# Performance work log

Hardware: AMD Instinct MI355X
Metric: run time of the kernel (lower is better)

The kernel has to match this reference:

```python
import jax, jax.numpy as jnp
import numpy as np

N, D, K = 262144, 64, 512


def setup_inputs() -> dict:
    key = jax.random.key(0)
    k1, k2 = jax.random.split(key)
    x = jax.random.normal(k1, (N, D), dtype=jnp.float32)
    # embedding initialized uniform(-1/K, 1/K) as in the torch module
    codebook = jax.random.uniform(k2, (K, D), dtype=jnp.float32, minval=-1.0 / K, maxval=1.0 / K)
    return {"x": x, "codebook": codebook}


def reference(x, codebook):
    # distances[n,k] = ||x_n||^2 + ||w_k||^2 - 2 x_n . w_k  (cdist^2 via matmul)
    d = (jnp.sum(x * x, axis=1, keepdims=True)
         + jnp.sum(codebook * codebook, axis=1)
         - 2.0 * jnp.matmul(x, codebook.T))  # [N, K]
    indices = jnp.argmin(d, axis=1)          # [N]
    x_q = codebook[indices]                  # [N, D] gather
    commitment_loss = jnp.mean((jax.lax.stop_gradient(x_q) - x) ** 2)
    embedding_loss = jnp.mean((x_q - jax.lax.stop_gradient(x)) ** 2)
    vq_loss = commitment_loss * 0.25 + embedding_loss
    # straight-through estimator
    x_out = x + jax.lax.stop_gradient(x_q - x)
    return (x_out, vq_loss)
```

## Files before the change

kernel.cpp:

```cpp
#include <hip/hip_runtime.h>
#include <hip/hip_bf16.h>
#include <hip/hip_fp8.h>

#define N_ROWS 262144
#define DIM    64
#define KCB    512

#define BLOCKS  1024
#define THREADS 512

typedef float f32x4 __attribute__((ext_vector_type(4)));

__device__ inline float dot4(float4 a) {
    return a.x * a.x + a.y * a.y + a.z * a.z + a.w * a.w;
}
__device__ inline unsigned umin2(unsigned a, unsigned b) { return a < b ? a : b; }

__device__ inline unsigned pk4(float a, float b, float c, float d) {
    unsigned r;
    r  = (unsigned)__hip_fp8_e4m3(a).__x;
    r |= (unsigned)__hip_fp8_e4m3(b).__x << 8;
    r |= (unsigned)__hip_fp8_e4m3(c).__x << 16;
    r |= (unsigned)__hip_fp8_e4m3(d).__x << 24;
    return r;
}
__device__ inline long pk8(float4 f0, float4 f1, float s) {
    unsigned lo = pk4(f0.x * s, f0.y * s, f0.z * s, f0.w * s);
    unsigned hi = pk4(f1.x * s, f1.y * s, f1.z * s, f1.w * s);
    return (long)(((unsigned long)hi << 32) | (unsigned long)lo);
}

__global__ __launch_bounds__(THREADS, 2) void vq_main(
    const float* __restrict__ x, const float* __restrict__ cb,
    float* __restrict__ out, float* __restrict__ partials)
{
    __shared__ long   cb8_sh[KCB * 8];
    __shared__ f32x4  wn_sh4[KCB / 4];
    __shared__ float  red_sh[8];

    const int tid    = threadIdx.x;
    const int lane   = tid & 63;
    const int wave   = tid >> 6;
    const int lane15 = lane & 15;
    const int half   = lane >> 4;

    const int wrow = blockIdx.x * 256 + wave * 32;
    const float* xc0 = x + (size_t)(wrow + lane15) * DIM + half * 8;
    const float* xc1 = x + (size_t)(wrow + 16 + lane15) * DIM + half * 8;

    float4 p00 = *(const float4*)xc0,        p01 = *(const float4*)(xc0 + 4);
    float4 p02 = *(const float4*)(xc0 + 32), p03 = *(const float4*)(xc0 + 36);
    float4 p10 = *(const float4*)xc1,        p11 = *(const float4*)(xc1 + 4);
    float4 p12 = *(const float4*)(xc1 + 32), p13 = *(const float4*)(xc1 + 36);

    #pragma unroll
    for (int it = 0; it < (KCB * 8) / THREADS; ++it) {
        const int fg = tid + it * THREADS;
        const int row = fg >> 3, g = fg & 7;
        const float* src = cb + row * DIM + g * 8;
        float4 f0 = *(const float4*)src;
        float4 f1 = *(const float4*)(src + 4);
        float sq = dot4(f0) + dot4(f1);
        sq += __shfl_xor(sq, 1);
        sq += __shfl_xor(sq, 2);
        sq += __shfl_xor(sq, 4);
        const int slot = ((row >> 1) << 4) + ((row & 1) << 3)
                       + (g ^ ((row >> 1) & 7));
        cb8_sh[slot] = pk8(f0, f1, -256.0f);
        if (g == 0) ((float*)wn_sh4)[row] = 256.0f + 128.0f * sq;
    }

    float xn0 = dot4(p00) + dot4(p01) + dot4(p02) + dot4(p03);
    float xn1 = dot4(p10) + dot4(p11) + dot4(p12) + dot4(p13);
    long b0lo = pk8(p00, p01, 1.0f), b0hi = pk8(p02, p03, 1.0f);
    long b1lo = pk8(p10, p11, 1.0f), b1hi = pk8(p12, p13, 1.0f);
    __syncthreads();

    const int key  = (lane15 >> 1) & 7;
    const int base = (lane15 >> 1) * 16 + (lane15 & 1) * 8;
    const int slo  = base + (half ^ key);
    const int shi  = slo ^ 4;
    const unsigned hb = (unsigned)(half * 4);

    unsigned u0 = 0xFFFFFFFFu, u1 = 0xFFFFFFFFu;

    #pragma unroll 8
    for (int t = 0; t < 32; ++t) {
        long  alo = cb8_sh[t * 128 + slo];
        long  ahi = cb8_sh[t * 128 + shi];
        f32x4 wnv = wn_sh4[t * 4 + half];
        const unsigned kb = (unsigned)(t * 16) | hb;

        f32x4 acc = wnv;
        acc = __builtin_amdgcn_mfma_f32_16x16x32_fp8_fp8(alo, b0lo, acc, 0, 0, 0);
        acc = __builtin_amdgcn_mfma_f32_16x16x32_fp8_fp8(ahi, b0hi, acc, 0, 0, 0);
        unsigned p0 = (__float_as_uint(acc[0]) & 0xFFFFFE00u) | kb;
        unsigned p1 = (__float_as_uint(acc[1]) & 0xFFFFFE00u) | (kb | 1u);
        unsigned p2 = (__float_as_uint(acc[2]) & 0xFFFFFE00u) | (kb | 2u);
        unsigned p3 = (__float_as_uint(acc[3]) & 0xFFFFFE00u) | (kb | 3u);
        u0 = umin2(u0, umin2(umin2(p0, p1), umin2(p2, p3)));

        f32x4 acd = wnv;
        acd = __builtin_amdgcn_mfma_f32_16x16x32_fp8_fp8(alo, b1lo, acd, 0, 0, 0);
        acd = __builtin_amdgcn_mfma_f32_16x16x32_fp8_fp8(ahi, b1hi, acd, 0, 0, 0);
        unsigned r0 = (__float_as_uint(acd[0]) & 0xFFFFFE00u) | kb;
        unsigned r1 = (__float_as_uint(acd[1]) & 0xFFFFFE00u) | (kb | 1u);
        unsigned r2 = (__float_as_uint(acd[2]) & 0xFFFFFE00u) | (kb | 2u);
        unsigned r3 = (__float_as_uint(acd[3]) & 0xFFFFFE00u) | (kb | 3u);
        u1 = umin2(u1, umin2(umin2(r0, r1), umin2(r2, r3)));
    }

    unsigned f0 = u0;
    f0 = umin2(f0, (unsigned)__shfl_xor((int)f0, 16));
    f0 = umin2(f0, (unsigned)__shfl_xor((int)f0, 32));
    unsigned f1 = u1;
    f1 = umin2(f1, (unsigned)__shfl_xor((int)f1, 16));
    f1 = umin2(f1, (unsigned)__shfl_xor((int)f1, 32));

    float xs0 = xn0;
    xs0 += __shfl_xor(xs0, 16); xs0 += __shfl_xor(xs0, 32);
    float xs1 = xn1;
    xs1 += __shfl_xor(xs1, 16); xs1 += __shfl_xor(xs1, 32);

    float pf0 = __uint_as_float(f0 & 0xFFFFFE00u);
    float pf1 = __uint_as_float(f1 & 0xFFFFFE00u);
    float lossAcc = 0.25f * (xs0 + pf0 * (1.0f / 128.0f) - 2.0f)
                  + 0.25f * (xs1 + pf1 * (1.0f / 128.0f) - 2.0f);

    const int bk0 = (int)(f0 & 511u);
    const int bk1 = (int)(f1 & 511u);

    float* outw = out + (size_t)wrow * DIM;
    #pragma unroll
    for (int j = 0; j < 8; ++j) {
        const int srcl = (j * 4 + half) & 15;
        int bk = __shfl((j >> 2) ? bk1 : bk0, srcl);
        float4 qv = *(const float4*)(cb + (size_t)bk * DIM + (lane & 15) * 4);
        *(float4*)(outw + j * 256 + lane * 4) = qv;
    }

    #pragma unroll
    for (int off = 1; off < 64; off <<= 1) lossAcc += __shfl_xor(lossAcc, off);
    if (lane == 0) red_sh[wave] = lossAcc;
    __syncthreads();
    if (tid == 0) {
        float s = 0.f;
        #pragma unroll
        for (int w = 0; w < 8; ++w) s += red_sh[w];
        partials[blockIdx.x] = s;
    }
}

__global__ void vq_finalize(const float* __restrict__ partials,
                            float* __restrict__ out_loss) {
    __shared__ float sh[256];
    int t = threadIdx.x;
    sh[t] = partials[t] + partials[t + 256] + partials[t + 512] + partials[t + 768];
    __syncthreads();
    #pragma unroll
    for (int s = 128; s > 0; s >>= 1) {
        if (t < s) sh[t] += sh[t + s];
        __syncthreads();
    }
    if (t == 0) out_loss[0] = sh[0] * (1.25f / (float)(N_ROWS * DIM));
}

extern "C" void kernel_launch(void* const* d_in, const int* in_sizes, int n_in,
                              void* d_out, int out_size, void* d_ws, size_t ws_size,
                              hipStream_t stream) {
    const float* x  = (const float*)d_in[0];
    const float* cb = (const float*)d_in[1];
    float* out      = (float*)d_out;
    float* partials = (float*)d_ws;

    hipLaunchKernelGGL(vq_main, dim3(BLOCKS), dim3(THREADS), 0, stream,
                       x, cb, out, partials);
    hipLaunchKernelGGL(vq_finalize, dim3(1), dim3(256), 0, stream,
                       partials, out + (size_t)N_ROWS * DIM);
}
```

Baseline: 44.80 us.

## Split VQ into score kernel writing indices and separate gather kernel

The fused kernel is split in two. The scoring kernel now writes only 16-bit argmin indices to workspace, and a new lightweight gather kernel writes the quantized rows to the output. The scoring loop handles its two 16-row chunks one after the other instead of interleaved, which lowers register pressure, and the second chunk's x loads are issued after the barrier so they overlap with the first chunk's compute. FP8 packing now uses the cvt_pk_fp8_f32 builtin. The cost is an extra kernel launch and an extra pass over the index buffer, plus less instruction-level parallelism in the MFMA loop.

```diff
diff --git a/kernel.cpp b/kernel.cpp
--- a/kernel.cpp
+++ b/kernel.cpp
@@ -1,13 +1,13 @@
 #include <hip/hip_runtime.h>
-#include <hip/hip_bf16.h>
-#include <hip/hip_fp8.h>
 
 #define N_ROWS 262144
 #define DIM    64
 #define KCB    512
 
-#define BLOCKS  1024
-#define THREADS 512
+#define ABLOCKS  1024
+#define ATHREADS 512
+#define BTHREADS 256
+#define BBLOCKS  ((N_ROWS * 16) / BTHREADS)
 
 typedef float f32x4 __attribute__((ext_vector_type(4)));
 
@@ -16,23 +16,18 @@
 }
 __device__ inline unsigned umin2(unsigned a, unsigned b) { return a < b ? a : b; }
 
-__device__ inline unsigned pk4(float a, float b, float c, float d) {
-    unsigned r;
-    r  = (unsigned)__hip_fp8_e4m3(a).__x;
-    r |= (unsigned)__hip_fp8_e4m3(b).__x << 8;
-    r |= (unsigned)__hip_fp8_e4m3(c).__x << 16;
-    r |= (unsigned)__hip_fp8_e4m3(d).__x << 24;
-    return r;
-}
 __device__ inline long pk8(float4 f0, float4 f1, float s) {
-    unsigned lo = pk4(f0.x * s, f0.y * s, f0.z * s, f0.w * s);
-    unsigned hi = pk4(f1.x * s, f1.y * s, f1.z * s, f1.w * s);
-    return (long)(((unsigned long)hi << 32) | (unsigned long)lo);
+    int lo = 0, hi = 0;
+    lo = __builtin_amdgcn_cvt_pk_fp8_f32(f0.x * s, f0.y * s, lo, false);
+    lo = __builtin_amdgcn_cvt_pk_fp8_f32(f0.z * s, f0.w * s, lo, true);
+    hi = __builtin_amdgcn_cvt_pk_fp8_f32(f1.x * s, f1.y * s, hi, false);
+    hi = __builtin_amdgcn_cvt_pk_fp8_f32(f1.z * s, f1.w * s, hi, true);
+    return (long)(((unsigned long)(unsigned)hi << 32) | (unsigned)lo);
 }
 
-__global__ __launch_bounds__(THREADS, 2) void vq_main(
+__global__ __launch_bounds__(ATHREADS, 2) void vq_score(
     const float* __restrict__ x, const float* __restrict__ cb,
-    float* __restrict__ out, float* __restrict__ partials)
+    unsigned short* __restrict__ idx, float* __restrict__ partials)
 {
     __shared__ long   cb8_sh[KCB * 8];
     __shared__ f32x4  wn_sh4[KCB / 4];
@@ -45,17 +40,14 @@
     const int half   = lane >> 4;
 
     const int wrow = blockIdx.x * 256 + wave * 32;
-    const float* xc0 = x + (size_t)(wrow + lane15) * DIM + half * 8;
-    const float* xc1 = x + (size_t)(wrow + 16 + lane15) * DIM + half * 8;
+    const float* xc = x + (size_t)(wrow + lane15) * DIM + half * 8;
 
-    float4 p00 = *(const float4*)xc0,        p01 = *(const float4*)(xc0 + 4);
-    float4 p02 = *(const float4*)(xc0 + 32), p03 = *(const float4*)(xc0 + 36);
-    float4 p10 = *(const float4*)xc1,        p11 = *(const float4*)(xc1 + 4);
-    float4 p12 = *(const float4*)(xc1 + 32), p13 = *(const float4*)(xc1 + 36);
+    float4 p00 = *(const float4*)xc,        p01 = *(const float4*)(xc + 4);
+    float4 p02 = *(const float4*)(xc + 32), p03 = *(const float4*)(xc + 36);
 
     #pragma unroll
-    for (int it = 0; it < (KCB * 8) / THREADS; ++it) {
-        const int fg = tid + it * THREADS;
+    for (int it = 0; it < (KCB * 8) / ATHREADS; ++it) {
+        const int fg = tid + it * ATHREADS;
         const int row = fg >> 3, g = fg & 7;
         const float* src = cb + row * DIM + g * 8;
         float4 f0 = *(const float4*)src;
@@ -71,72 +63,59 @@
     }
 
     float xn0 = dot4(p00) + dot4(p01) + dot4(p02) + dot4(p03);
-    float xn1 = dot4(p10) + dot4(p11) + dot4(p12) + dot4(p13);
     long b0lo = pk8(p00, p01, 1.0f), b0hi = pk8(p02, p03, 1.0f);
-    long b1lo = pk8(p10, p11, 1.0f), b1hi = pk8(p12, p13, 1.0f);
     __syncthreads();
+
+    float4 q00 = *(const float4*)(xc + 1024), q01 = *(const float4*)(xc + 1028);
+    float4 q02 = *(const float4*)(xc + 1056), q03 = *(const float4*)(xc + 1060);
 
     const int key  = (lane15 >> 1) & 7;
     const int base = (lane15 >> 1) * 16 + (lane15 & 1) * 8;
     const int slo  = base + (half ^ key);
     const int shi  = slo ^ 4;
-    const unsigned hb = (unsigned)(half * 4);
+    const unsigned hb   = (unsigned)(half * 4);
+    const unsigned mask = 0xFFFFFE00u;
 
-    unsigned u0 = 0xFFFFFFFFu, u1 = 0xFFFFFFFFu;
+    float lossAcc = 0.f;
+    long blo = b0lo, bhi = b0hi;
+    float xn = xn0;
 
-    #pragma unroll 8
-    for (int t = 0; t < 32; ++t) {
-        long  alo = cb8_sh[t * 128 + slo];
-        long  ahi = cb8_sh[t * 128 + shi];
-        f32x4 wnv = wn_sh4[t * 4 + half];
-        const unsigned kb = (unsigned)(t * 16) | hb;
+    #pragma unroll
+    for (int ch = 0; ch < 2; ++ch) {
+        if (ch == 1) {
+            xn  = dot4(q00) + dot4(q01) + dot4(q02) + dot4(q03);
+            blo = pk8(q00, q01, 1.0f);
+            bhi = pk8(q02, q03, 1.0f);
+        }
+        unsigned u0 = 0xFFFFFFFFu;
 
-        f32x4 acc = wnv;
-        acc = __builtin_amdgcn_mfma_f32_16x16x32_fp8_fp8(alo, b0lo, acc, 0, 0, 0);
-        acc = __builtin_amdgcn_mfma_f32_16x16x32_fp8_fp8(ahi, b0hi, acc, 0, 0, 0);
-        unsigned p0 = (__float_as_uint(acc[0]) & 0xFFFFFE00u) | kb;
-        unsigned p1 = (__float_as_uint(acc[1]) & 0xFFFFFE00u) | (kb | 1u);
-        unsigned p2 = (__float_as_uint(acc[2]) & 0xFFFFFE00u) | (kb | 2u);
-        unsigned p3 = (__float_as_uint(acc[3]) & 0xFFFFFE00u) | (kb | 3u);
-        u0 = umin2(u0, umin2(umin2(p0, p1), umin2(p2, p3)));
+        #pragma unroll 8
+        for (int t = 0; t < 32; ++t) {
+            long  alo = cb8_sh[t * 128 + slo];
+            long  ahi = cb8_sh[t * 128 + shi];
+            f32x4 wnv = wn_sh4[t * 4 + half];
+            const unsigned kb = (unsigned)(t * 16) | hb;
 
-        f32x4 acd = wnv;
-        acd = __builtin_amdgcn_mfma_f32_16x16x32_fp8_fp8(alo, b1lo, acd, 0, 0, 0);
-        acd = __builtin_amdgcn_mfma_f32_16x16x32_fp8_fp8(ahi, b1hi, acd, 0, 0, 0);
-        unsigned r0 = (__float_as_uint(acd[0]) & 0xFFFFFE00u) | kb;
-        unsigned r1 = (__float_as_uint(acd[1]) & 0xFFFFFE00u) | (kb | 1u);
-        unsigned r2 = (__float_as_uint(acd[2]) & 0xFFFFFE00u) | (kb | 2u);
-        unsigned r3 = (__float_as_uint(acd[3]) & 0xFFFFFE00u) | (kb | 3u);
-        u1 = umin2(u1, umin2(umin2(r0, r1), umin2(r2, r3)));
-    }
+            f32x4 acc = wnv;
+            acc = __builtin_amdgcn_mfma_f32_16x16x32_fp8_fp8(alo, blo, acc, 0, 0, 0);
+            acc = __builtin_amdgcn_mfma_f32_16x16x32_fp8_fp8(ahi, bhi, acc, 0, 0, 0);
+            unsigned p0 = (__float_as_uint(acc[0]) & mask) | kb;
+            unsigned p1 = (__float_as_uint(acc[1]) & mask) | (kb | 1u);
+            unsigned p2 = (__float_as_uint(acc[2]) & mask) | (kb | 2u);
+            unsigned p3 = (__float_as_uint(acc[3]) & mask) | (kb | 3u);
+            u0 = umin2(u0, umin2(umin2(p0, p1), umin2(p2, p3)));
+        }
 
-    unsigned f0 = u0;
-    f0 = umin2(f0, (unsigned)__shfl_xor((int)f0, 16));
-    f0 = umin2(f0, (unsigned)__shfl_xor((int)f0, 32));
-    unsigned f1 = u1;
-    f1 = umin2(f1, (unsigned)__shfl_xor((int)f1, 16));
-    f1 = umin2(f1, (unsigned)__shfl_xor((int)f1, 32));
+        unsigned f0 = u0;
+        f0 = umin2(f0, (unsigned)__shfl_xor((int)f0, 16));
+        f0 = umin2(f0, (unsigned)__shfl_xor((int)f0, 32));
+        float xs = xn;
+        xs += __shfl_xor(xs, 16); xs += __shfl_xor(xs, 32);
 
-    float xs0 = xn0;
-    xs0 += __shfl_xor(xs0, 16); xs0 += __shfl_xor(xs0, 32);
-    float xs1 = xn1;
-    xs1 += __shfl_xor(xs1, 16); xs1 += __shfl_xor(xs1, 32);
+        float pf = __uint_as_float(f0 & mask);
+        lossAcc += 0.25f * (xs + pf * (1.0f / 128.0f) - 2.0f);
 
-    float pf0 = __uint_as_float(f0 & 0xFFFFFE00u);
-    float pf1 = __uint_as_float(f1 & 0xFFFFFE00u);
-    float lossAcc = 0.25f * (xs0 + pf0 * (1.0f / 128.0f) - 2.0f)
-                  + 0.25f * (xs1 + pf1 * (1.0f / 128.0f) - 2.0f);
-
-    const int bk0 = (int)(f0 & 511u);
-    const int bk1 = (int)(f1 & 511u);
-
-    float* outw = out + (size_t)wrow * DIM;
-    #pragma unroll
-    for (int j = 0; j < 8; ++j) {
-        const int srcl = (j * 4 + half) & 15;
-        int bk = __shfl((j >> 2) ? bk1 : bk0, srcl);
-        float4 qv = *(const float4*)(cb + (size_t)bk * DIM + (lane & 15) * 4);
-        *(float4*)(outw + j * 256 + lane * 4) = qv;
+        if (lane < 16) idx[wrow + ch * 16 + lane] = (unsigned short)(f0 & 511u);
     }
 
     #pragma unroll
@@ -149,6 +128,18 @@
         for (int w = 0; w < 8; ++w) s += red_sh[w];
         partials[blockIdx.x] = s;
     }
+}
+
+__global__ __launch_bounds__(BTHREADS, 8) void vq_gather(
+    const unsigned short* __restrict__ idx, const float* __restrict__ cb,
+    float* __restrict__ out)
+{
+    const int g   = blockIdx.x * BTHREADS + threadIdx.x;
+    const int row = g >> 4;
+    const int dq  = g & 15;
+    const int k   = (int)idx[row];
+    const f32x4* cb4 = (const f32x4*)cb;
+    ((f32x4*)out)[g] = cb4[k * 16 + dq];
 }
 
 __global__ void vq_finalize(const float* __restrict__ partials,
@@ -172,9 +163,12 @@
     const float* cb = (const float*)d_in[1];
     float* out      = (float*)d_out;
     float* partials = (float*)d_ws;
+    unsigned short* idx = (unsigned short*)((char*)d_ws + 4096);
 
-    hipLaunchKernelGGL(vq_main, dim3(BLOCKS), dim3(THREADS), 0, stream,
-                       x, cb, out, partials);
+    hipLaunchKernelGGL(vq_score, dim3(ABLOCKS), dim3(ATHREADS), 0, stream,
+                       x, cb, idx, partials);
+    hipLaunchKernelGGL(vq_gather, dim3(BBLOCKS), dim3(BTHREADS), 0, stream,
+                       idx, cb, out);
     hipLaunchKernelGGL(vq_finalize, dim3(1), dim3(256), 0, stream,
                        partials, out + (size_t)N_ROWS * DIM);
 }
```

Result: slower. 48.16 us (+7.5%).
